# Performance work log

Hardware: AMD Instinct MI355X
Metric: run time of the kernel (lower is better)

Reference implementation:

```python
import jax, jax.numpy as jnp
import numpy as np

N, HEADS, OUT = 8192, 4, 64  # hidden = HEADS*OUT = 256
DIN = 256
NEG = -9e15
ALPHA = 0.2


def setup_inputs() -> dict:
    key = jax.random.key(0)
    ks = jax.random.split(key, 6)
    X = jax.random.normal(ks[0], (N, DIN), dtype=jnp.float32)
    A = jax.random.randint(ks[1], (N, N), 0, 2, dtype=jnp.int32)  # dense 0/1 adjacency
    hid = HEADS * OUT
    W = jax.random.normal(ks[2], (hid, DIN), dtype=jnp.float32) * 0.05  # nn.Linear weight [out,in]
    b = jax.random.normal(ks[3], (hid,), dtype=jnp.float32) * 0.05
    a_s = jax.random.normal(ks[4], (hid, 1), dtype=jnp.float32) * 0.05
    a_r = jax.random.normal(ks[5], (hid, 1), dtype=jnp.float32) * 0.05
    return {"X": X, "A": A, "W": W, "b": b, "a_s": a_s, "a_r": a_r}


def reference(X, A, W, b, a_s, a_r):
    Af = A.astype(jnp.float32)
    H_in = X @ W.T + b                      # [N, hid]
    s = H_in @ a_s                          # [N, 1]
    r = H_in @ a_r                          # [N, 1]
    M = Af * s + Af * r.T                   # M_s + M_r, [N, N]
    scores = jax.nn.leaky_relu(M, negative_slope=ALPHA)
    masked = jnp.where(Af > 0, scores, jnp.float32(NEG))
    C = jax.nn.softmax(masked, axis=1)      # row softmax; dropout = identity (eval)
    H_out = C @ H_in                        # [N, hid]; act = Identity, LayerNorm output discarded
    H_final = H_out.reshape(N, HEADS, OUT).sum(axis=1)  # concat='sum'
    return H_final
```

## Files before the change

kernel.cpp:

```cpp
#include <hip/hip_runtime.h>

typedef __attribute__((ext_vector_type(8))) short short8;
typedef __attribute__((ext_vector_type(4))) short short4v;
typedef __attribute__((ext_vector_type(4))) float f32x4;
typedef __attribute__((ext_vector_type(4))) int i32x4;

#define NN 8192
#define ALPHA 0.2f

__device__ __forceinline__ float bf16_to_f32(unsigned short h) {
    union { unsigned int u; float f; } c;
    c.u = ((unsigned int)h) << 16;
    return c.f;
}
__device__ __forceinline__ unsigned short f32_to_bf16(float f) {
    union { float f; unsigned int u; } c;
    c.f = f;
    unsigned int r = (c.u + 0x7FFFu + ((c.u >> 16) & 1u)) >> 16;
    return (unsigned short)r;
}
__device__ __forceinline__ unsigned short f32_to_bf16_fast(float f) {
    union { float f; unsigned int u; } c;
    c.f = f;
    return (unsigned short)((c.u + 0x8000u) >> 16);
}

__device__ __forceinline__ int probe_isbf16(const void* Xv, int tid) {
    __shared__ int wsum[4];
    const unsigned short* x16 = (const unsigned short*)Xv;
    int cnt = 0;
#pragma unroll
    for (int j = 0; j < 4; j++) {
        float v = bf16_to_f32(x16[tid * 4 + j]);
        float a = fabsf(v);
        if (a > 1e-6f && a < 64.0f) cnt++;
    }
#pragma unroll
    for (int m = 1; m <= 32; m <<= 1) cnt += __shfl_xor(cnt, m, 64);
    if ((tid & 63) == 0) wsum[tid >> 6] = cnt;
    __syncthreads();
    return (wsum[0] + wsum[1] + wsum[2] + wsum[3]) > 800;
}

__global__ __launch_bounds__(256) void gat_prep(
    const void* __restrict__ Xv, const void* __restrict__ Wv,
    const void* __restrict__ bv, const void* __restrict__ asv,
    const void* __restrict__ arv,
    short* __restrict__ Xb, short* __restrict__ Wb,
    float* __restrict__ bF, float* __restrict__ asF, float* __restrict__ arF,
    int* __restrict__ flagOut) {
    const int tid = threadIdx.x;
    const int isBf = probe_isbf16(Xv, tid);
    if (blockIdx.x == 0 && tid == 0) *flagOut = isBf;

    const int GX = NN * 256 / 8;
    const int GW = 256 * 256 / 8;
    const int idx = blockIdx.x * 256 + tid;
    const int stride = 256 * 256;
    for (int i = idx; i < GX + GW; i += stride) {
        const void* src = (i < GX) ? Xv : Wv;
        short* dst = (i < GX) ? Xb : Wb;
        int g = (i < GX) ? i : i - GX;
        short8 o;
        if (isBf) {
            o = ((const short8*)src)[g];
        } else {
            f32x4 a = ((const f32x4*)src)[2 * g];
            f32x4 b = ((const f32x4*)src)[2 * g + 1];
#pragma unroll
            for (int j = 0; j < 4; j++) {
                o[j] = (short)f32_to_bf16(a[j]);
                o[4 + j] = (short)f32_to_bf16(b[j]);
            }
        }
        ((short8*)dst)[g] = o;
    }
    if (idx < 768) {
        int which = idx >> 8;
        int k = idx & 255;
        const void* src = (which == 0) ? bv : (which == 1) ? asv : arv;
        float v = isBf ? bf16_to_f32(((const unsigned short*)src)[k])
                       : ((const float*)src)[k];
        float* dst = (which == 0) ? bF : (which == 1) ? asF : arF;
        dst[k] = v;
    }
}

__global__ __launch_bounds__(128) void gat_gemm1(
    const short* __restrict__ Xb, const short* __restrict__ Wb,
    const float* __restrict__ bF, const float* __restrict__ asF,
    const float* __restrict__ arF,
    short* __restrict__ Gfrag, float* __restrict__ sOut, float* __restrict__ rOut) {
    __shared__ short Gl[64][32];
    const int tid = threadIdx.x;
    const int wave = tid >> 6, lane = tid & 63;
    const int l15 = lane & 15, lhi = lane >> 4;
    const int rowBase = blockIdx.x * 32 + wave * 16;

    f32x4 acc[16];
#pragma unroll
    for (int n = 0; n < 16; n++) acc[n] = (f32x4){0.f, 0.f, 0.f, 0.f};

    const short8* Xrow = (const short8*)(Xb + (size_t)(rowBase + l15) * 256);
#pragma unroll
    for (int ks = 0; ks < 8; ks++) {
        short8 a = Xrow[ks * 4 + lhi];
#pragma unroll
        for (int n = 0; n < 16; n++) {
            const short8* Wrow = (const short8*)(Wb + (size_t)(n * 16 + l15) * 256);
            short8 bf = Wrow[ks * 4 + lhi];
            acc[n] = __builtin_amdgcn_mfma_f32_16x16x32_bf16(a, bf, acc[n], 0, 0, 0);
        }
    }

    float sPart[4] = {0.f, 0.f, 0.f, 0.f};
    float rPart[4] = {0.f, 0.f, 0.f, 0.f};
    float g[4][4];
#pragma unroll
    for (int na = 0; na < 4; na++)
#pragma unroll
        for (int q = 0; q < 4; q++) g[na][q] = 0.f;

#pragma unroll
    for (int n = 0; n < 16; n++) {
        int col = n * 16 + l15;
        float bias = bF[col], asc = asF[col], arc = arF[col];
#pragma unroll
        for (int q = 0; q < 4; q++) {
            float h = acc[n][q] + bias;
            sPart[q] += h * asc;
            rPart[q] += h * arc;
            g[n & 3][q] += h;
        }
    }

#pragma unroll
    for (int na = 0; na < 4; na++)
#pragma unroll
        for (int q = 0; q < 4; q++)
            Gl[na * 16 + l15][wave * 16 + lhi * 4 + q] = (short)f32_to_bf16(g[na][q]);

#pragma unroll
    for (int m = 1; m <= 8; m <<= 1) {
#pragma unroll
        for (int q = 0; q < 4; q++) {
            sPart[q] += __shfl_xor(sPart[q], m, 64);
            rPart[q] += __shfl_xor(rPart[q], m, 64);
        }
    }
    if (l15 == 0) {
#pragma unroll
        for (int q = 0; q < 4; q++) {
            int row = rowBase + lhi * 4 + q;
            sOut[row] = sPart[q];
            rOut[row] = rPart[q];
        }
    }

    __syncthreads();
    const int t_ = blockIdx.x >> 1, h_ = blockIdx.x & 1;
#pragma unroll
    for (int e = tid; e < 256; e += 128) {
        int n_ = e >> 6, le = e & 63;
        short8 v = *(const short8*)(&Gl[n_ * 16 + (le & 15)][(le >> 4) * 8]);
        *(short8*)(Gfrag + ((size_t)t_ * 8 + h_ * 4 + n_) * 512 + le * 8) = v;
    }
}


#define GAT_LOADA(S0, S1, S2, S3, AB_, T_)                                   \
    {                                                                        \
        const int* p_ = (AB_) + (size_t)(T_) * 64;                           \
        S0 = *(const i32x4*)(p_);                                            \
        S1 = *(const i32x4*)(p_ + NN);                                       \
        S2 = *(const i32x4*)(p_ + 2 * NN);                                   \
        S3 = *(const i32x4*)(p_ + 3 * NN);                                   \
    }

#define GAT_BAL(Q0, Q1, Q2, Q3, V0, V1, V2, V3)                              \
    {                                                                        \
        unsigned long long W00 = __ballot((V0)[0] != 0);                     \
        unsigned long long W01 = __ballot((V0)[1] != 0);                     \
        unsigned long long W02 = __ballot((V0)[2] != 0);                     \
        unsigned long long W03 = __ballot((V0)[3] != 0);                     \
        unsigned long long W10 = __ballot((V1)[0] != 0);                     \
        unsigned long long W11 = __ballot((V1)[1] != 0);                     \
        unsigned long long W12 = __ballot((V1)[2] != 0);                     \
        unsigned long long W13 = __ballot((V1)[3] != 0);                     \
        unsigned long long W20 = __ballot((V2)[0] != 0);                     \
        unsigned long long W21 = __ballot((V2)[1] != 0);                     \
        unsigned long long W22 = __ballot((V2)[2] != 0);                     \
        unsigned long long W23 = __ballot((V2)[3] != 0);                     \
        unsigned long long W30 = __ballot((V3)[0] != 0);                     \
        unsigned long long W31 = __ballot((V3)[1] != 0);                     \
        unsigned long long W32 = __ballot((V3)[2] != 0);                     \
        unsigned long long W33 = __ballot((V3)[3] != 0);                     \
        unsigned long long w0_ = r3 == 0 ? W00 : r3 == 1 ? W10               \
                               : r3 == 2 ? W20 : W30;                        \
        unsigned long long w1_ = r3 == 0 ? W01 : r3 == 1 ? W11               \
                               : r3 == 2 ? W21 : W31;                        \
        unsigned long long w2_ = r3 == 0 ? W02 : r3 == 1 ? W12               \
                               : r3 == 2 ? W22 : W32;                        \
        unsigned long long w3_ = r3 == 0 ? W03 : r3 == 1 ? W13               \
                               : r3 == 2 ? W23 : W33;                        \
        Q0 = (unsigned int)(w0_ >> shBase);                                  \
        Q1 = (unsigned int)(w1_ >> shBase);                                  \
        Q2 = (unsigned int)(w2_ >> shBase);                                  \
        Q3 = (unsigned int)(w3_ >> shBase);                                  \
    }

#define GAT_ELEM(PA_, JP_, XV_, TW_, SH_)                                    \
    {                                                                        \
        float x_ = (XV_);                                                    \
        x_ = fmaxf(x_, ALPHA * x_);                                          \
        float e_ = __expf(x_);                                               \
        PA_[JP_] = ((TW_ >> (SH_)) & 1u) ? (short)f32_to_bf16_fast(e_)       \
                                         : (short)0;                         \
    }

#define GAT_PA(PAH0, PAH1, SM_, Q0, Q1, Q2, Q3)                              \
    {                                                                        \
        GAT_ELEM(PAH0, 0, (SM_) + ra0[0], Q0, 0)                             \
        GAT_ELEM(PAH0, 1, (SM_) + ra0[1], Q1, 0)                             \
        GAT_ELEM(PAH0, 2, (SM_) + ra0[2], Q2, 0)                             \
        GAT_ELEM(PAH0, 3, (SM_) + ra0[3], Q3, 0)                             \
        GAT_ELEM(PAH0, 4, (SM_) + ra1[0], Q0, 1)                             \
        GAT_ELEM(PAH0, 5, (SM_) + ra1[1], Q1, 1)                             \
        GAT_ELEM(PAH0, 6, (SM_) + ra1[2], Q2, 1)                             \
        GAT_ELEM(PAH0, 7, (SM_) + ra1[3], Q3, 1)                             \
        GAT_ELEM(PAH1, 0, (SM_) + rb0[0], Q0, 8)                             \
        GAT_ELEM(PAH1, 1, (SM_) + rb0[1], Q1, 8)                             \
        GAT_ELEM(PAH1, 2, (SM_) + rb0[2], Q2, 8)                             \
        GAT_ELEM(PAH1, 3, (SM_) + rb0[3], Q3, 8)                             \
        GAT_ELEM(PAH1, 4, (SM_) + rb1[0], Q0, 9)                             \
        GAT_ELEM(PAH1, 5, (SM_) + rb1[1], Q1, 9)                             \
        GAT_ELEM(PAH1, 6, (SM_) + rb1[2], Q2, 9)                             \
        GAT_ELEM(PAH1, 7, (SM_) + rb1[3], Q3, 9)                             \
    }

#define GAT_MFMA_HALF(H_)                                                    \
    {                                                                        \
        const short* bp_ = Gfrag + ((size_t)ktg * 8 + (H_) * 4) * 512 +      \
                           lane * 8;                                         \
        short8 bv0 = *(const short8*)(bp_);                                  \
        short8 bv1 = *(const short8*)(bp_ + 512);                            \
        short8 bv2 = *(const short8*)(bp_ + 1024);                           \
        short8 bv3 = *(const short8*)(bp_ + 1536);                           \
        acc[0][0] = __builtin_amdgcn_mfma_f32_16x16x32_bf16(pa0[H_], bv0,    \
                                                            acc[0][0], 0, 0, 0); \
        acc[0][1] = __builtin_amdgcn_mfma_f32_16x16x32_bf16(pa0[H_], bv1,    \
                                                            acc[0][1], 0, 0, 0); \
        acc[0][2] = __builtin_amdgcn_mfma_f32_16x16x32_bf16(pa0[H_], bv2,    \
                                                            acc[0][2], 0, 0, 0); \
        acc[0][3] = __builtin_amdgcn_mfma_f32_16x16x32_bf16(pa0[H_], bv3,    \
                                                            acc[0][3], 0, 0, 0); \
        acc[0][4] = __builtin_amdgcn_mfma_f32_16x16x32_bf16(pa0[H_], onesB,  \
                                                            acc[0][4], 0, 0, 0); \
        acc[1][0] = __builtin_amdgcn_mfma_f32_16x16x32_bf16(pa1[H_], bv0,    \
                                                            acc[1][0], 0, 0, 0); \
        acc[1][1] = __builtin_amdgcn_mfma_f32_16x16x32_bf16(pa1[H_], bv1,    \
                                                            acc[1][1], 0, 0, 0); \
        acc[1][2] = __builtin_amdgcn_mfma_f32_16x16x32_bf16(pa1[H_], bv2,    \
                                                            acc[1][2], 0, 0, 0); \
        acc[1][3] = __builtin_amdgcn_mfma_f32_16x16x32_bf16(pa1[H_], bv3,    \
                                                            acc[1][3], 0, 0, 0); \
        acc[1][4] = __builtin_amdgcn_mfma_f32_16x16x32_bf16(pa1[H_], onesB,  \
                                                            acc[1][4], 0, 0, 0); \
    }

__global__ __launch_bounds__(256, 3) void gat_pv8(
    const int* __restrict__ A, const short* __restrict__ Gfrag,
    const float* __restrict__ sV, const float* __restrict__ rV,
    float* __restrict__ accP, float* __restrict__ denP) {
    __shared__ float Ls[4][32][68];
    __shared__ float Ld[4][32];

    const int tid = threadIdx.x;
    const int wave = tid >> 6, lane = tid & 63;
    const int l15 = lane & 15, lhi = lane >> 4;
    const int rb = blockIdx.x / 3;
    const int ks3 = blockIdx.x - rb * 3;
    const int i0 = rb * 32;
    const int tstart = ks3 * 43;
    const int tcnt = (ks3 < 2) ? 43 : 42;

    const int r3 = l15 & 3;
    const int shBase = ((l15 >> 2) << 4) + (lhi << 1);

    const float s0m = sV[i0 + l15];
    const float s1m = sV[i0 + 16 + l15];
    const int* ab0 = A + (size_t)(i0 + lhi * 4) * NN + l15 * 4;
    const int* ab1 = ab0 + (size_t)16 * NN;
    const float* rvb = rV + lhi * 8;

    short8 onesB;
#pragma unroll
    for (int j = 0; j < 8; j++) onesB[j] = (l15 == 0) ? (short)0x3F80 : (short)0;

    f32x4 acc[2][5];
#pragma unroll
    for (int rg = 0; rg < 2; rg++)
#pragma unroll
        for (int n = 0; n < 5; n++) acc[rg][n] = (f32x4){0.f, 0.f, 0.f, 0.f};

    i32x4 s00, s01, s02, s03, s10, s11, s12, s13;
    GAT_LOADA(s00, s01, s02, s03, ab0, tstart + wave);
    GAT_LOADA(s10, s11, s12, s13, ab1, tstart + wave);

    for (int tt = wave; tt < tcnt; tt += 4) {
        const int ktg = tstart + tt;
        const int k0 = ktg * 64;
        f32x4 ra0 = *(const f32x4*)(rvb + k0);
        f32x4 ra1 = *(const f32x4*)(rvb + k0 + 4);
        f32x4 rb0 = *(const f32x4*)(rvb + k0 + 32);
        f32x4 rb1 = *(const f32x4*)(rvb + k0 + 36);

        unsigned int q00, q01, q02, q03, q10, q11, q12, q13;
        GAT_BAL(q00, q01, q02, q03, s00, s01, s02, s03);
        GAT_BAL(q10, q11, q12, q13, s10, s11, s12, s13);

        const int tn = (tt + 4 < tcnt) ? ktg + 4 : ktg;
        GAT_LOADA(s00, s01, s02, s03, ab0, tn);
        GAT_LOADA(s10, s11, s12, s13, ab1, tn);

        short8 pa0[2], pa1[2];
        GAT_PA(pa0[0], pa0[1], s0m, q00, q01, q02, q03);
        GAT_PA(pa1[0], pa1[1], s1m, q10, q11, q12, q13);

        GAT_MFMA_HALF(0);
        GAT_MFMA_HALF(1);
    }

#pragma unroll
    for (int rg = 0; rg < 2; rg++)
#pragma unroll
        for (int n = 0; n < 4; n++)
#pragma unroll
            for (int q = 0; q < 4; q++)
                Ls[wave][rg * 16 + lhi * 4 + q][n * 16 + l15] = acc[rg][n][q];
    if (l15 == 0) {
#pragma unroll
        for (int rg = 0; rg < 2; rg++)
#pragma unroll
            for (int q = 0; q < 4; q++)
                Ld[wave][rg * 16 + lhi * 4 + q] = acc[rg][4][q];
    }
    __syncthreads();

    const int row = tid >> 3, c0 = (tid & 7) * 8;
    float v[8];
#pragma unroll
    for (int j = 0; j < 8; j++)
        v[j] = Ls[0][row][c0 + j] + Ls[1][row][c0 + j] +
               Ls[2][row][c0 + j] + Ls[3][row][c0 + j];
    float* aout = accP + (size_t)ks3 * NN * 64 + (size_t)(i0 + row) * 64 + c0;
    *(f32x4*)aout = (f32x4){v[0], v[1], v[2], v[3]};
    *((f32x4*)aout + 1) = (f32x4){v[4], v[5], v[6], v[7]};
    if (tid < 32)
        denP[(size_t)ks3 * NN + i0 + tid] =
            Ld[0][tid] + Ld[1][tid] + Ld[2][tid] + Ld[3][tid];
}

__global__ void gat_final(const float* __restrict__ accP, const float* __restrict__ denP,
                          const int* __restrict__ flag, void* __restrict__ outP) {
    int idx = blockIdx.x * blockDim.x + threadIdx.x;
    if (idx >= NN * 16) return;
    int row = idx >> 4;
    float den = 0.f;
    f32x4 v = (f32x4){0.f, 0.f, 0.f, 0.f};
#pragma unroll
    for (int sk = 0; sk < 3; sk++) {
        den += denP[(size_t)sk * NN + row];
        f32x4 a = *((const f32x4*)(accP + (size_t)sk * NN * 64) + idx);
        v.x += a.x; v.y += a.y; v.z += a.z; v.w += a.w;
    }
    float inv = 1.0f / den;
    v.x *= inv; v.y *= inv; v.z *= inv; v.w *= inv;
    if (*flag) {
        short4v pk;
#pragma unroll
        for (int j = 0; j < 4; j++) pk[j] = (short)f32_to_bf16(v[j]);
        *((short4v*)outP + idx) = pk;
    } else {
        *((f32x4*)outP + idx) = v;
    }
}

extern "C" void kernel_launch(void* const* d_in, const int* in_sizes, int n_in,
                              void* d_out, int out_size, void* d_ws, size_t ws_size,
                              hipStream_t stream) {
    const void* X  = d_in[0];
    const int*  A  = (const int*)d_in[1];
    const void* W  = d_in[2];
    const void* bb = d_in[3];
    const void* as_ = d_in[4];
    const void* ar_ = d_in[5];

    char* ws = (char*)d_ws;
    const size_t OFF_FLAG = 0;
    const size_t OFF_XB   = 256;
    const size_t OFF_WB   = OFF_XB + (size_t)NN * 256 * 2;
    const size_t OFF_BF   = OFF_WB + (size_t)256 * 256 * 2;
    const size_t OFF_ASF  = OFF_BF + 1024;
    const size_t OFF_ARF  = OFF_ASF + 1024;
    const size_t OFF_S    = OFF_ARF + 1024;
    const size_t OFF_R    = OFF_S + (size_t)NN * 4;
    const size_t OFF_GF   = OFF_R + (size_t)NN * 4;
    const size_t OFF_ACC  = OFF_GF + (size_t)64 * NN * 2;
    const size_t OFF_DEN  = OFF_ACC + (size_t)3 * NN * 64 * 4;

    int*   flag = (int*)(ws + OFF_FLAG);
    short* Xb   = (short*)(ws + OFF_XB);
    short* Wb   = (short*)(ws + OFF_WB);
    float* bF   = (float*)(ws + OFF_BF);
    float* asF  = (float*)(ws + OFF_ASF);
    float* arF  = (float*)(ws + OFF_ARF);
    float* sP   = (float*)(ws + OFF_S);
    float* rP   = (float*)(ws + OFF_R);
    short* Gf   = (short*)(ws + OFF_GF);
    float* accP = (float*)(ws + OFF_ACC);
    float* denP = (float*)(ws + OFF_DEN);

    gat_prep<<<256, 256, 0, stream>>>(X, W, bb, as_, ar_, Xb, Wb, bF, asF, arF, flag);
    gat_gemm1<<<NN / 32, 128, 0, stream>>>(Xb, Wb, bF, asF, arF, Gf, sP, rP);
    gat_pv8<<<256 * 3, 256, 0, stream>>>(A, Gf, sP, rP, accP, denP);
    gat_final<<<NN * 16 / 256, 256, 0, stream>>>(accP, denP, flag, d_out);
}
```

Baseline: 79.75 us.

## Double-buffer adjacency and G-fragment loads with split-K of two

The attention-times-values kernel now splits the K dimension into two halves instead of three, using 512 blocks with launch bounds lowered to two blocks per CU. The main loop is manually unrolled with two register buffer sets, so both the adjacency tile and the G fragments for the next step are prefetched while the current step's ballots and MFMAs run. The final reduction is adjusted to sum two partials. This is meant to hide global-load latency and reduce partial-sum traffic, at the cost of many more registers and lower occupancy.

```diff
diff --git a/kernel.cpp b/kernel.cpp
--- a/kernel.cpp
+++ b/kernel.cpp
@@ -168,13 +168,31 @@
 }
 
 
-#define GAT_LOADA(S0, S1, S2, S3, AB_, T_)                                   \
-    {                                                                        \
-        const int* p_ = (AB_) + (size_t)(T_) * 64;                           \
-        S0 = *(const i32x4*)(p_);                                            \
-        S1 = *(const i32x4*)(p_ + NN);                                       \
-        S2 = *(const i32x4*)(p_ + 2 * NN);                                   \
-        S3 = *(const i32x4*)(p_ + 3 * NN);                                   \
+#define GAT_LOADA(AR, T_)                                                    \
+    {                                                                        \
+        const int* pA0_ = ab0 + (size_t)(T_) * 64;                           \
+        const int* pA1_ = ab1 + (size_t)(T_) * 64;                           \
+        AR[0] = *(const i32x4*)(pA0_);                                       \
+        AR[1] = *(const i32x4*)(pA0_ + NN);                                  \
+        AR[2] = *(const i32x4*)(pA0_ + 2 * NN);                              \
+        AR[3] = *(const i32x4*)(pA0_ + 3 * NN);                              \
+        AR[4] = *(const i32x4*)(pA1_);                                       \
+        AR[5] = *(const i32x4*)(pA1_ + NN);                                  \
+        AR[6] = *(const i32x4*)(pA1_ + 2 * NN);                              \
+        AR[7] = *(const i32x4*)(pA1_ + 3 * NN);                              \
+    }
+
+#define GAT_LOADG(GR, T_)                                                    \
+    {                                                                        \
+        const short* bp_ = Gfrag + (size_t)(T_) * 4096 + lane * 8;           \
+        GR[0] = *(const short8*)(bp_);                                       \
+        GR[1] = *(const short8*)(bp_ + 512);                                 \
+        GR[2] = *(const short8*)(bp_ + 1024);                                \
+        GR[3] = *(const short8*)(bp_ + 1536);                                \
+        GR[4] = *(const short8*)(bp_ + 2048);                                \
+        GR[5] = *(const short8*)(bp_ + 2560);                                \
+        GR[6] = *(const short8*)(bp_ + 3072);                                \
+        GR[7] = *(const short8*)(bp_ + 3584);                                \
     }
 
 #define GAT_BAL(Q0, Q1, Q2, Q3, V0, V1, V2, V3)                              \
@@ -238,37 +256,62 @@
         GAT_ELEM(PAH1, 7, (SM_) + rb1[3], Q3, 9)                             \
     }
 
-#define GAT_MFMA_HALF(H_)                                                    \
-    {                                                                        \
-        const short* bp_ = Gfrag + ((size_t)ktg * 8 + (H_) * 4) * 512 +      \
-                           lane * 8;                                         \
-        short8 bv0 = *(const short8*)(bp_);                                  \
-        short8 bv1 = *(const short8*)(bp_ + 512);                            \
-        short8 bv2 = *(const short8*)(bp_ + 1024);                           \
-        short8 bv3 = *(const short8*)(bp_ + 1536);                           \
-        acc[0][0] = __builtin_amdgcn_mfma_f32_16x16x32_bf16(pa0[H_], bv0,    \
+#define GAT_BODY(TT_, AR, GR)                                                \
+    {                                                                        \
+        const int k0_ = (tstart + (TT_)) * 64;                               \
+        f32x4 ra0 = *(const f32x4*)(rvb + k0_);                              \
+        f32x4 ra1 = *(const f32x4*)(rvb + k0_ + 4);                          \
+        f32x4 rb0 = *(const f32x4*)(rvb + k0_ + 32);                         \
+        f32x4 rb1 = *(const f32x4*)(rvb + k0_ + 36);                         \
+        unsigned int q00, q01, q02, q03, q10, q11, q12, q13;                 \
+        GAT_BAL(q00, q01, q02, q03, AR[0], AR[1], AR[2], AR[3]);             \
+        GAT_BAL(q10, q11, q12, q13, AR[4], AR[5], AR[6], AR[7]);             \
+        short8 pa0[2], pa1[2];                                               \
+        GAT_PA(pa0[0], pa0[1], s0m, q00, q01, q02, q03);                     \
+        GAT_PA(pa1[0], pa1[1], s1m, q10, q11, q12, q13);                     \
+        acc[0][0] = __builtin_amdgcn_mfma_f32_16x16x32_bf16(pa0[0], GR[0],   \
                                                             acc[0][0], 0, 0, 0); \
-        acc[0][1] = __builtin_amdgcn_mfma_f32_16x16x32_bf16(pa0[H_], bv1,    \
+        acc[0][1] = __builtin_amdgcn_mfma_f32_16x16x32_bf16(pa0[0], GR[1],   \
                                                             acc[0][1], 0, 0, 0); \
-        acc[0][2] = __builtin_amdgcn_mfma_f32_16x16x32_bf16(pa0[H_], bv2,    \
+        acc[0][2] = __builtin_amdgcn_mfma_f32_16x16x32_bf16(pa0[0], GR[2],   \
                                                             acc[0][2], 0, 0, 0); \
-        acc[0][3] = __builtin_amdgcn_mfma_f32_16x16x32_bf16(pa0[H_], bv3,    \
+        acc[0][3] = __builtin_amdgcn_mfma_f32_16x16x32_bf16(pa0[0], GR[3],   \
                                                             acc[0][3], 0, 0, 0); \
-        acc[0][4] = __builtin_amdgcn_mfma_f32_16x16x32_bf16(pa0[H_], onesB,  \
+        acc[0][4] = __builtin_amdgcn_mfma_f32_16x16x32_bf16(pa0[0], onesB,   \
                                                             acc[0][4], 0, 0, 0); \
-        acc[1][0] = __builtin_amdgcn_mfma_f32_16x16x32_bf16(pa1[H_], bv0,    \
+        acc[1][0] = __builtin_amdgcn_mfma_f32_16x16x32_bf16(pa1[0], GR[0],   \
                                                             acc[1][0], 0, 0, 0); \
-        acc[1][1] = __builtin_amdgcn_mfma_f32_16x16x32_bf16(pa1[H_], bv1,    \
+        acc[1][1] = __builtin_amdgcn_mfma_f32_16x16x32_bf16(pa1[0], GR[1],   \
                                                             acc[1][1], 0, 0, 0); \
-        acc[1][2] = __builtin_amdgcn_mfma_f32_16x16x32_bf16(pa1[H_], bv2,    \
+        acc[1][2] = __builtin_amdgcn_mfma_f32_16x16x32_bf16(pa1[0], GR[2],   \
                                                             acc[1][2], 0, 0, 0); \
-        acc[1][3] = __builtin_amdgcn_mfma_f32_16x16x32_bf16(pa1[H_], bv3,    \
+        acc[1][3] = __builtin_amdgcn_mfma_f32_16x16x32_bf16(pa1[0], GR[3],   \
                                                             acc[1][3], 0, 0, 0); \
-        acc[1][4] = __builtin_amdgcn_mfma_f32_16x16x32_bf16(pa1[H_], onesB,  \
+        acc[1][4] = __builtin_amdgcn_mfma_f32_16x16x32_bf16(pa1[0], onesB,   \
                                                             acc[1][4], 0, 0, 0); \
-    }
-
-__global__ __launch_bounds__(256, 3) void gat_pv8(
+        acc[0][0] = __builtin_amdgcn_mfma_f32_16x16x32_bf16(pa0[1], GR[4],   \
+                                                            acc[0][0], 0, 0, 0); \
+        acc[0][1] = __builtin_amdgcn_mfma_f32_16x16x32_bf16(pa0[1], GR[5],   \
+                                                            acc[0][1], 0, 0, 0); \
+        acc[0][2] = __builtin_amdgcn_mfma_f32_16x16x32_bf16(pa0[1], GR[6],   \
+                                                            acc[0][2], 0, 0, 0); \
+        acc[0][3] = __builtin_amdgcn_mfma_f32_16x16x32_bf16(pa0[1], GR[7],   \
+                                                            acc[0][3], 0, 0, 0); \
+        acc[0][4] = __builtin_amdgcn_mfma_f32_16x16x32_bf16(pa0[1], onesB,   \
+                                                            acc[0][4], 0, 0, 0); \
+        acc[1][0] = __builtin_amdgcn_mfma_f32_16x16x32_bf16(pa1[1], GR[4],   \
+                                                            acc[1][0], 0, 0, 0); \
+        acc[1][1] = __builtin_amdgcn_mfma_f32_16x16x32_bf16(pa1[1], GR[5],   \
+                                                            acc[1][1], 0, 0, 0); \
+        acc[1][2] = __builtin_amdgcn_mfma_f32_16x16x32_bf16(pa1[1], GR[6],   \
+                                                            acc[1][2], 0, 0, 0); \
+        acc[1][3] = __builtin_amdgcn_mfma_f32_16x16x32_bf16(pa1[1], GR[7],   \
+                                                            acc[1][3], 0, 0, 0); \
+        acc[1][4] = __builtin_amdgcn_mfma_f32_16x16x32_bf16(pa1[1], onesB,   \
+                                                            acc[1][4], 0, 0, 0); \
+    }
+
+__global__ __launch_bounds__(256, 2) void gat_pv9(
     const int* __restrict__ A, const short* __restrict__ Gfrag,
     const float* __restrict__ sV, const float* __restrict__ rV,
     float* __restrict__ accP, float* __restrict__ denP) {
@@ -278,18 +321,17 @@
     const int tid = threadIdx.x;
     const int wave = tid >> 6, lane = tid & 63;
     const int l15 = lane & 15, lhi = lane >> 4;
-    const int rb = blockIdx.x / 3;
-    const int ks3 = blockIdx.x - rb * 3;
+    const int rb = blockIdx.x >> 1;
+    const int ks2 = blockIdx.x & 1;
     const int i0 = rb * 32;
-    const int tstart = ks3 * 43;
-    const int tcnt = (ks3 < 2) ? 43 : 42;
+    const int tstart = ks2 * 64;
 
     const int r3 = l15 & 3;
     const int shBase = ((l15 >> 2) << 4) + (lhi << 1);
 
     const float s0m = sV[i0 + l15];
     const float s1m = sV[i0 + 16 + l15];
-    const int* ab0 = A + (size_t)(i0 + lhi * 4) * NN + l15 * 4;
+    const int* ab0 = A + (size_t)(i0 + lhi * 4) * NN + l15 * 4 + (size_t)tstart * 64;
     const int* ab1 = ab0 + (size_t)16 * NN;
     const float* rvb = rV + lhi * 8;
 
@@ -303,32 +345,27 @@
 #pragma unroll
         for (int n = 0; n < 5; n++) acc[rg][n] = (f32x4){0.f, 0.f, 0.f, 0.f};
 
-    i32x4 s00, s01, s02, s03, s10, s11, s12, s13;
-    GAT_LOADA(s00, s01, s02, s03, ab0, tstart + wave);
-    GAT_LOADA(s10, s11, s12, s13, ab1, tstart + wave);
-
-    for (int tt = wave; tt < tcnt; tt += 4) {
-        const int ktg = tstart + tt;
-        const int k0 = ktg * 64;
-        f32x4 ra0 = *(const f32x4*)(rvb + k0);
-        f32x4 ra1 = *(const f32x4*)(rvb + k0 + 4);
-        f32x4 rb0 = *(const f32x4*)(rvb + k0 + 32);
-        f32x4 rb1 = *(const f32x4*)(rvb + k0 + 36);
-
-        unsigned int q00, q01, q02, q03, q10, q11, q12, q13;
-        GAT_BAL(q00, q01, q02, q03, s00, s01, s02, s03);
-        GAT_BAL(q10, q11, q12, q13, s10, s11, s12, s13);
-
-        const int tn = (tt + 4 < tcnt) ? ktg + 4 : ktg;
-        GAT_LOADA(s00, s01, s02, s03, ab0, tn);
-        GAT_LOADA(s10, s11, s12, s13, ab1, tn);
-
-        short8 pa0[2], pa1[2];
-        GAT_PA(pa0[0], pa0[1], s0m, q00, q01, q02, q03);
-        GAT_PA(pa1[0], pa1[1], s1m, q10, q11, q12, q13);
-
-        GAT_MFMA_HALF(0);
-        GAT_MFMA_HALF(1);
+    i32x4 aA[8], aB[8];
+    short8 gA[8], gB[8];
+    int tt = wave;
+    GAT_LOADA(aA, tt);
+    GAT_LOADG(gA, tstart + tt);
+    while (tt < 64) {
+        {
+            const int tn = (tt + 4 < 64) ? tt + 4 : tt;
+            GAT_LOADA(aB, tn);
+            GAT_LOADG(gB, tstart + tn);
+        }
+        GAT_BODY(tt, aA, gA);
+        tt += 4;
+        if (tt >= 64) break;
+        {
+            const int tn = (tt + 4 < 64) ? tt + 4 : tt;
+            GAT_LOADA(aA, tn);
+            GAT_LOADG(gA, tstart + tn);
+        }
+        GAT_BODY(tt, aB, gB);
+        tt += 4;
     }
 
 #pragma unroll
@@ -353,11 +390,11 @@
     for (int j = 0; j < 8; j++)
         v[j] = Ls[0][row][c0 + j] + Ls[1][row][c0 + j] +
                Ls[2][row][c0 + j] + Ls[3][row][c0 + j];
-    float* aout = accP + (size_t)ks3 * NN * 64 + (size_t)(i0 + row) * 64 + c0;
+    float* aout = accP + (size_t)ks2 * NN * 64 + (size_t)(i0 + row) * 64 + c0;
     *(f32x4*)aout = (f32x4){v[0], v[1], v[2], v[3]};
     *((f32x4*)aout + 1) = (f32x4){v[4], v[5], v[6], v[7]};
     if (tid < 32)
-        denP[(size_t)ks3 * NN + i0 + tid] =
+        denP[(size_t)ks2 * NN + i0 + tid] =
             Ld[0][tid] + Ld[1][tid] + Ld[2][tid] + Ld[3][tid];
 }
 
@@ -369,7 +406,7 @@
     float den = 0.f;
     f32x4 v = (f32x4){0.f, 0.f, 0.f, 0.f};
 #pragma unroll
-    for (int sk = 0; sk < 3; sk++) {
+    for (int sk = 0; sk < 2; sk++) {
         den += denP[(size_t)sk * NN + row];
         f32x4 a = *((const f32x4*)(accP + (size_t)sk * NN * 64) + idx);
         v.x += a.x; v.y += a.y; v.z += a.z; v.w += a.w;
@@ -407,7 +444,7 @@
     const size_t OFF_R    = OFF_S + (size_t)NN * 4;
     const size_t OFF_GF   = OFF_R + (size_t)NN * 4;
     const size_t OFF_ACC  = OFF_GF + (size_t)64 * NN * 2;
-    const size_t OFF_DEN  = OFF_ACC + (size_t)3 * NN * 64 * 4;
+    const size_t OFF_DEN  = OFF_ACC + (size_t)2 * NN * 64 * 4;
 
     int*   flag = (int*)(ws + OFF_FLAG);
     short* Xb   = (short*)(ws + OFF_XB);
@@ -423,6 +460,6 @@
 
     gat_prep<<<256, 256, 0, stream>>>(X, W, bb, as_, ar_, Xb, Wb, bF, asF, arF, flag);
     gat_gemm1<<<NN / 32, 128, 0, stream>>>(Xb, Wb, bF, asF, arF, Gf, sP, rP);
-    gat_pv8<<<256 * 3, 256, 0, stream>>>(A, Gf, sP, rP, accP, denP);
+    gat_pv9<<<256 * 2, 256, 0, stream>>>(A, Gf, sP, rP, accP, denP);
     gat_final<<<NN * 16 / 256, 256, 0, stream>>>(accP, denP, flag, d_out);
 }
```

Measured after the change: 89.17 us. 1.12x slower.
